# Kernel tuning notes

Measured on AMD Instinct MI355X. Metric: run time of the kernel, lower is better.

## Reference

```python
import jax, jax.numpy as jnp
import numpy as np
import math

D_MODEL = 1024
N_HEADS = 16
SLOT_DIM = 64
N_SLOTS = 1024
TOP_K = 2
LN_EPS = 1e-5


def setup_inputs() -> dict:
    key = jax.random.key(0)
    ks = jax.random.split(key, 8)
    x = jax.random.normal(ks[0], (4, 2048, D_MODEL), dtype=jnp.float32)
    ln_gamma = jnp.ones((D_MODEL,), jnp.float32)
    ln_beta = jnp.zeros((D_MODEL,), jnp.float32)
    q_w = jax.random.normal(ks[1], (N_HEADS * SLOT_DIM, D_MODEL), jnp.float32) / math.sqrt(D_MODEL)
    q_b = jnp.zeros((N_HEADS * SLOT_DIM,), jnp.float32)
    slot_signatures = jax.random.normal(ks[2], (N_HEADS, N_SLOTS, SLOT_DIM), jnp.float32) * 0.5
    slot_values = jax.random.normal(ks[3], (N_HEADS, N_SLOTS, SLOT_DIM), jnp.float32) * 0.02
    out_w = jax.random.normal(ks[4], (D_MODEL, N_HEADS * SLOT_DIM), jnp.float32) / math.sqrt(N_HEADS * SLOT_DIM)
    out_b = jnp.zeros((D_MODEL,), jnp.float32)
    temperature = jnp.ones((1,), jnp.float32)
    return {"x": x, "ln_gamma": ln_gamma, "ln_beta": ln_beta, "q_w": q_w, "q_b": q_b,
            "slot_signatures": slot_signatures, "slot_values": slot_values,
            "out_w": out_w, "out_b": out_b, "temperature": temperature}


def _ternary_ste(sig):
    # forward = {-1,0,+1} quantization; backward = identity (straight-through)
    q = jnp.where(sig > 0.3, 1.0, jnp.where(sig < -0.3, -1.0, 0.0))
    return sig + jax.lax.stop_gradient(q - sig)


def reference(x, ln_gamma, ln_beta, q_w, q_b, slot_signatures, slot_values, out_w, out_b, temperature):
    B, T, D = x.shape
    # LayerNorm
    mean = jnp.mean(x, axis=-1, keepdims=True)
    var = jnp.var(x, axis=-1, keepdims=True)
    x_norm = (x - mean) * jax.lax.rsqrt(var + LN_EPS) * ln_gamma + ln_beta
    # Query projection -> [B, T, H, slot_dim]
    q = (x_norm @ q_w.T + q_b).reshape(B, T, N_HEADS, SLOT_DIM)
    sigs = _ternary_ste(slot_signatures)  # [H, S, d]
    scores = jnp.einsum('bthd,hsd->bths', q, sigs)
    scores = scores / (temperature * math.sqrt(SLOT_DIM))  # [B, T, H, S]
    # top-k routing
    topk_scores, slot_idx = jax.lax.top_k(scores, TOP_K)  # [B, T, H, K]
    weights = jax.nn.softmax(topk_scores, axis=-1)
    # gather selected slot values: [B, T, H, K, d]
    h_idx = jnp.arange(N_HEADS)[None, None, :, None]
    selected = slot_values[h_idx, slot_idx]
    read = jnp.sum(selected * weights[..., None], axis=3)  # [B, T, H, d]
    read = read.reshape(B, T, N_HEADS * SLOT_DIM)
    out = read @ out_w.T + out_b
    return x + out
```

## Files before the change

kernel.cpp:

```cpp
#include <hip/hip_runtime.h>

typedef unsigned short u16;
typedef unsigned int   u32;
typedef float f32x4  __attribute__((ext_vector_type(4)));
typedef __bf16 bf16x8 __attribute__((ext_vector_type(8)));

__device__ __forceinline__ u16 f2bf(float f){
  u32 u = __float_as_uint(f);
  u += 0x7fffu + ((u >> 16) & 1u);
  return (u16)(u >> 16);
}

__device__ __forceinline__ void gld16(const void* g, void* l){
  __builtin_amdgcn_global_load_lds((const __attribute__((address_space(1))) u32*)g,
                                   (__attribute__((address_space(3))) u32*)l, 16, 0, 0);
}

__global__ __launch_bounds__(256) void convert_kernel(
    const float* __restrict__ qw, const float* __restrict__ ow,
    const float* __restrict__ sg,
    u16* __restrict__ qwb, u16* __restrict__ owb, u16* __restrict__ sgb){
  int i = (blockIdx.x * 256 + threadIdx.x) * 4;
  f32x4 a = *(const f32x4*)(qw + i);
  f32x4 b = *(const f32x4*)(ow + i);
  f32x4 s = *(const f32x4*)(sg + i);
  uint2 pa, pb, ps;
  pa.x = (u32)f2bf(a[0]) | ((u32)f2bf(a[1]) << 16);
  pa.y = (u32)f2bf(a[2]) | ((u32)f2bf(a[3]) << 16);
  pb.x = (u32)f2bf(b[0]) | ((u32)f2bf(b[1]) << 16);
  pb.y = (u32)f2bf(b[2]) | ((u32)f2bf(b[3]) << 16);
  float t0 = (s[0] > 0.3f) ? 1.0f : ((s[0] < -0.3f) ? -1.0f : 0.0f);
  float t1 = (s[1] > 0.3f) ? 1.0f : ((s[1] < -0.3f) ? -1.0f : 0.0f);
  float t2 = (s[2] > 0.3f) ? 1.0f : ((s[2] < -0.3f) ? -1.0f : 0.0f);
  float t3 = (s[3] > 0.3f) ? 1.0f : ((s[3] < -0.3f) ? -1.0f : 0.0f);
  ps.x = (u32)f2bf(t0) | ((u32)f2bf(t1) << 16);
  ps.y = (u32)f2bf(t2) | ((u32)f2bf(t3) << 16);
  *(uint2*)(qwb + i) = pa;
  *(uint2*)(owb + i) = pb;
  *(uint2*)(sgb + i) = ps;
}

__global__ __launch_bounds__(256) void ln_kernel(
    const float* __restrict__ x, const float* __restrict__ g,
    const float* __restrict__ b, u16* __restrict__ xn){
  const int t = blockIdx.x, tid = threadIdx.x;
  f32x4 v = *(const f32x4*)(x + (size_t)t * 1024 + tid * 4);
  float s  = v[0] + v[1] + v[2] + v[3];
  float ss = v[0]*v[0] + v[1]*v[1] + v[2]*v[2] + v[3]*v[3];
  for (int off = 32; off; off >>= 1){
    s  += __shfl_down(s, off);
    ss += __shfl_down(ss, off);
  }
  __shared__ float red[8];
  int w = tid >> 6;
  if ((tid & 63) == 0){ red[w] = s; red[4 + w] = ss; }
  __syncthreads();
  s  = red[0] + red[1] + red[2] + red[3];
  ss = red[4] + red[5] + red[6] + red[7];
  float mean = s * (1.0f / 1024.0f);
  float var  = ss * (1.0f / 1024.0f) - mean * mean;
  float rs   = rsqrtf(var + 1e-5f);
  f32x4 gv = *(const f32x4*)(g + tid * 4);
  f32x4 bv = *(const f32x4*)(b + tid * 4);
  float y0 = (v[0]-mean)*rs*gv[0]+bv[0];
  float y1 = (v[1]-mean)*rs*gv[1]+bv[1];
  float y2 = (v[2]-mean)*rs*gv[2]+bv[2];
  float y3 = (v[3]-mean)*rs*gv[3]+bv[3];
  uint2 pk;
  pk.x = (u32)f2bf(y0) | ((u32)f2bf(y1) << 16);
  pk.y = (u32)f2bf(y2) | ((u32)f2bf(y3) << 16);
  *(uint2*)(xn + (size_t)t * 1024 + tid * 4) = pk;
}

__global__ __launch_bounds__(256, 2) void gemm_bt(
    const u16* __restrict__ A, const u16* __restrict__ B,
    const float* __restrict__ bias, const float* __restrict__ resid,
    float* __restrict__ outf, u16* __restrict__ outb, int mode){
  __shared__ u16 As[2][128 * 64];
  __shared__ u16 Bs[2][128 * 64];
  const int tid = threadIdx.x;
  const int b = blockIdx.x;
  const int m0 = ((b & 7) * 8 + ((b >> 3) & 7)) * 128;
  const int n0 = (b >> 6) * 128;
  const int w = tid >> 6, lane = tid & 63, lm = lane & 15, quad = lane >> 4;
  const int wm = (w & 1) * 64, wn = (w >> 1) * 64;
  const int lr = lane >> 3;
  const int lg = (lane & 7) ^ lr;
  const f32x4 fz = {0.f, 0.f, 0.f, 0.f};
  f32x4 acc[4][4];
  #pragma unroll
  for (int i = 0; i < 4; ++i)
    #pragma unroll
    for (int j = 0; j < 4; ++j) acc[i][j] = fz;

  const u16* gA = A + (size_t)(m0 + w * 32 + lr) * 1024 + lg * 8;
  const u16* gB = B + (size_t)(n0 + w * 32 + lr) * 1024 + lg * 8;
  const int lbase = (w * 32) * 64;
  const int sw = lm & 7;

  auto stage = [&](int kt, int bb){
    #pragma unroll
    for (int sub = 0; sub < 4; ++sub){
      gld16(gA + (size_t)(sub * 8) * 1024 + kt * 64, &As[bb][lbase + sub * 8 * 64]);
      gld16(gB + (size_t)(sub * 8) * 1024 + kt * 64, &Bs[bb][lbase + sub * 8 * 64]);
    }
  };

  stage(0, 0);
  for (int kt = 0; kt < 16; ++kt){
    __syncthreads();
    if (kt < 15) stage(kt + 1, (kt + 1) & 1);
    const u16* as = As[kt & 1];
    const u16* bs = Bs[kt & 1];
    #pragma unroll
    for (int kk = 0; kk < 2; ++kk){
      const int ch = ((quad + kk * 4) ^ sw) * 8;
      bf16x8 afr[4], bfr[4];
      #pragma unroll
      for (int i = 0; i < 4; ++i)
        afr[i] = *(const bf16x8*)(&as[(wm + i * 16 + lm) * 64 + ch]);
      #pragma unroll
      for (int j = 0; j < 4; ++j)
        bfr[j] = *(const bf16x8*)(&bs[(wn + j * 16 + lm) * 64 + ch]);
      #pragma unroll
      for (int i = 0; i < 4; ++i)
        #pragma unroll
        for (int j = 0; j < 4; ++j)
          acc[i][j] = __builtin_amdgcn_mfma_f32_16x16x32_bf16(afr[i], bfr[j], acc[i][j], 0, 0, 0);
    }
  }

  #pragma unroll
  for (int i = 0; i < 4; ++i){
    #pragma unroll
    for (int r = 0; r < 4; ++r){
      int grow = m0 + wm + i * 16 + quad * 4 + r;
      #pragma unroll
      for (int j = 0; j < 4; ++j){
        int gcol = n0 + wn + j * 16 + lm;
        float v = acc[i][j][r] + bias[gcol];
        if (mode){
          v += resid[(size_t)grow * 1024 + gcol];
          outf[(size_t)grow * 1024 + gcol] = v;
        } else {
          outb[(size_t)grow * 1024 + gcol] = f2bf(v);
        }
      }
    }
  }
}

__global__ __launch_bounds__(256) void route_kernel(
    const u16* __restrict__ q, const u16* __restrict__ sig,
    const float* __restrict__ V, const float* __restrict__ temp,
    u16* __restrict__ rd){
  const int h = blockIdx.y;
  const int t0 = blockIdx.x * 128;
  const int tid = threadIdx.x, w = tid >> 6, lane = tid & 63;
  const int lm = lane & 15, quad = lane >> 4;

  __shared__ u16 sbuf[2][128 * 64];
  __shared__ float fw1[128], fw2[128];
  __shared__ int   fi1[128], fi2[128];

  const u16* q0 = q + (size_t)(t0 + w * 32 + lm) * 1024 + h * 64 + quad * 8;
  bf16x8 qf00 = *(const bf16x8*)(q0);
  bf16x8 qf01 = *(const bf16x8*)(q0 + 32);
  bf16x8 qf10 = *(const bf16x8*)(q0 + 16 * 1024);
  bf16x8 qf11 = *(const bf16x8*)(q0 + 16 * 1024 + 32);

  const u16* sigh = sig + (size_t)h * 65536;

  const int lr = lane >> 3, lg = (lane & 7) ^ lr;
  const u16* ssrc = sigh + (size_t)(w * 32 + lr) * 64 + lg * 8;
  auto stage = [&](int t, int bb){
    const u16* s0 = ssrc + (size_t)t * 128 * 64;
    u16* d0 = &sbuf[bb][(w * 32) * 64];
    #pragma unroll
    for (int sub = 0; sub < 4; ++sub)
      gld16(s0 + sub * 8 * 64, d0 + sub * 8 * 64);
  };

  const int base1 = lm * 64 + ((quad ^ (lm & 7)) * 8);
  const int base2 = base1 ^ 32;

  const f32x4 fz4 = {0.f, 0.f, 0.f, 0.f};
  const u32 vq = (u32)(quad * 4);
  float v1a = -3.0e38f, v2a = -3.0e38f, v1b = -3.0e38f, v2b = -3.0e38f;
  u32 b1a = 0, b2a = 0, b1b = 0, b2b = 0;

  stage(0, 0);
  for (int t = 0; t < 8; ++t){
    __syncthreads();
    if (t < 7) stage(t + 1, (t + 1) & 1);
    const u16* buf = sbuf[t & 1];
    #pragma unroll
    for (int g = 0; g < 8; ++g){
      bf16x8 s1 = *(const bf16x8*)(&buf[g * 1024 + base1]);
      bf16x8 s2 = *(const bf16x8*)(&buf[g * 1024 + base2]);
      u32 bt = (u32)(t * 8 + g);
      #pragma unroll
      for (int set = 0; set < 2; ++set){
        f32x4 acc = __builtin_amdgcn_mfma_f32_16x16x32_bf16(s1, set ? qf10 : qf00, fz4, 0, 0, 0);
        acc       = __builtin_amdgcn_mfma_f32_16x16x32_bf16(s2, set ? qf11 : qf01, acc, 0, 0, 0);
        float k0 = __uint_as_float((__float_as_uint(acc[0]) & 0xFFFFFFF0u) | vq);
        float k1 = __uint_as_float((__float_as_uint(acc[1]) & 0xFFFFFFF0u) | (vq + 1u));
        float k2 = __uint_as_float((__float_as_uint(acc[2]) & 0xFFFFFFF0u) | (vq + 2u));
        float k3 = __uint_as_float((__float_as_uint(acc[3]) & 0xFFFFFFF0u) | (vq + 3u));
        float h1 = fmaxf(k0, k1), h2 = fminf(k0, k1);
        float h3 = fmaxf(k2, k3), h4 = fminf(k2, k3);
        float m1 = fmaxf(h1, h3);
        float m2 = __builtin_amdgcn_fmed3f(h1, h3, fmaxf(h2, h4));
        float v1 = set ? v1b : v1a, v2 = set ? v2b : v2a;
        u32   b1 = set ? b1b : b1a, b2 = set ? b2b : b2a;
        u32   cb2 = (m2 > v2) ? bt : b2;
        float c2  = fmaxf(v2, m2);
        u32   nb1 = (m1 > v1) ? bt : b1;
        float n1  = fmaxf(v1, m1);
        float n2  = __builtin_amdgcn_fmed3f(v1, m1, c2);
        u32   nb2 = (n2 == m1) ? bt : ((n2 == v1) ? b1 : cb2);
        if (set){ v1b = n1; b1b = nb1; v2b = n2; b2b = nb2; }
        else    { v1a = n1; b1a = nb1; v2a = n2; b2a = nb2; }
      }
    }
  }

  #pragma unroll
  for (int off = 16; off <= 32; off <<= 1){
    #pragma unroll
    for (int set = 0; set < 2; ++set){
      float v1 = set ? v1b : v1a, v2 = set ? v2b : v2a;
      u32   b1 = set ? b1b : b1a, b2 = set ? b2b : b2a;
      float o1 = __shfl_xor(v1, off);
      float o2 = __shfl_xor(v2, off);
      u32 ob1 = (u32)__shfl_xor((int)b1, off);
      u32 ob2 = (u32)__shfl_xor((int)b2, off);
      u32   cb2 = (o2 > v2) ? ob2 : b2;
      float c2  = fmaxf(v2, o2);
      u32   nb1 = (o1 > v1) ? ob1 : b1;
      float n1  = fmaxf(v1, o1);
      float n2  = __builtin_amdgcn_fmed3f(v1, o1, c2);
      u32   nb2 = (n2 == o1) ? ob1 : ((n2 == v1) ? b1 : cb2);
      if (set){ v1b = n1; b1b = nb1; v2b = n2; b2b = nb2; }
      else    { v1a = n1; b1a = nb1; v2a = n2; b2a = nb2; }
    }
  }

  if (quad == 0){
    float tsc = 1.0f / (temp[0] * 8.0f);
    #pragma unroll
    for (int set = 0; set < 2; ++set){
      float v1 = set ? v1b : v1a, v2 = set ? v2b : v2a;
      u32   b1 = set ? b1b : b1a, b2 = set ? b2b : b2a;
      int tl = w * 32 + set * 16 + lm;
      u32 u1 = __float_as_uint(v1);
      u32 u2 = __float_as_uint(v2);
      float s1 = __uint_as_float(u1 & 0xFFFFFFF0u);
      float s2 = __uint_as_float(u2 & 0xFFFFFFF0u);
      float ex = __expf((s2 - s1) * tsc);
      float iw = 1.0f / (1.0f + ex);
      fw1[tl] = iw; fw2[tl] = ex * iw;
      fi1[tl] = (int)(b1 * 16 + (u1 & 15u));
      fi2[tl] = (int)(b2 * 16 + (u2 & 15u));
    }
  }
  __syncthreads();

  int tl = tid >> 1, d0 = (tid & 1) * 32;
  const float* va = V + ((size_t)h * 1024 + fi1[tl]) * 64 + d0;
  const float* vb = V + ((size_t)h * 1024 + fi2[tl]) * 64 + d0;
  float W1 = fw1[tl], W2 = fw2[tl];
  u16* dst = rd + (size_t)(t0 + tl) * 1024 + h * 64 + d0;
  #pragma unroll
  for (int g = 0; g < 4; ++g){
    f32x4 xa = *(const f32x4*)(va + g * 8);
    f32x4 xb = *(const f32x4*)(va + g * 8 + 4);
    f32x4 ya = *(const f32x4*)(vb + g * 8);
    f32x4 yb = *(const f32x4*)(vb + g * 8 + 4);
    uint4 o;
    o.x = (u32)f2bf(W1*xa[0]+W2*ya[0]) | ((u32)f2bf(W1*xa[1]+W2*ya[1]) << 16);
    o.y = (u32)f2bf(W1*xa[2]+W2*ya[2]) | ((u32)f2bf(W1*xa[3]+W2*ya[3]) << 16);
    o.z = (u32)f2bf(W1*xb[0]+W2*yb[0]) | ((u32)f2bf(W1*xb[1]+W2*yb[1]) << 16);
    o.w = (u32)f2bf(W1*xb[2]+W2*yb[2]) | ((u32)f2bf(W1*xb[3]+W2*yb[3]) << 16);
    *(uint4*)(dst + g * 8) = o;
  }
}

extern "C" void kernel_launch(void* const* d_in, const int* in_sizes, int n_in,
                              void* d_out, int out_size, void* d_ws, size_t ws_size,
                              hipStream_t stream){
  const float* x    = (const float*)d_in[0];
  const float* lng  = (const float*)d_in[1];
  const float* lnb  = (const float*)d_in[2];
  const float* qw   = (const float*)d_in[3];
  const float* qb   = (const float*)d_in[4];
  const float* sig  = (const float*)d_in[5];
  const float* sv   = (const float*)d_in[6];
  const float* ow   = (const float*)d_in[7];
  const float* ob   = (const float*)d_in[8];
  const float* temp = (const float*)d_in[9];
  float* out = (float*)d_out;

  char* ws = (char*)d_ws;
  u16* xn   = (u16*)(ws);
  u16* qwb  = (u16*)(ws + 16777216);
  u16* owb  = (u16*)(ws + 16777216 + 2097152);
  u16* sgb  = (u16*)(ws + 16777216 + 2 * 2097152);
  u16* qb16 = (u16*)(ws + 16777216 + 3 * 2097152);
  u16* rdb  = xn;

  convert_kernel<<<1024, 256, 0, stream>>>(qw, ow, sig, qwb, owb, sgb);
  ln_kernel<<<8192, 256, 0, stream>>>(x, lng, lnb, xn);
  gemm_bt<<<512, 256, 0, stream>>>(xn, qwb, qb, nullptr, nullptr, qb16, 0);
  route_kernel<<<dim3(64, 16), 256, 0, stream>>>(qb16, sgb, sv, temp, rdb);
  gemm_bt<<<512, 256, 0, stream>>>(rdb, owb, ob, x, out, nullptr, 1);
}
```

Baseline: 217.1 us.

## Split route slots across waves with 32x32 MFMA and make LayerNorm one wave per row

The routing kernel now gives each wave its own quarter of the slots for 64 tokens, using 32x32x16 bf16 MFMAs. Each wave streams its slots through a private double buffer, synchronized with waitcnt instead of block barriers. The per-wave top-2 results are merged across waves through shared memory before the gather. LayerNorm handles one row per wave using xor-shuffle reductions, which removes the shared-memory reduction and the barrier. The trade-off is more route blocks and a cross-wave merge step, and correctness now depends on the manual waitcnt encodings.

```diff
diff --git a/kernel.cpp b/kernel.cpp
--- a/kernel.cpp
+++ b/kernel.cpp
@@ -3,6 +3,7 @@
 typedef unsigned short u16;
 typedef unsigned int   u32;
 typedef float f32x4  __attribute__((ext_vector_type(4)));
+typedef float f32x16 __attribute__((ext_vector_type(16)));
 typedef __bf16 bf16x8 __attribute__((ext_vector_type(8)));
 
 __device__ __forceinline__ u16 f2bf(float f){
@@ -15,6 +16,10 @@
   __builtin_amdgcn_global_load_lds((const __attribute__((address_space(1))) u32*)g,
                                    (__attribute__((address_space(3))) u32*)l, 16, 0, 0);
 }
+
+#define WAITCNT_VM0   0x0F70
+#define WAITCNT_VM4   0x0F74
+#define WAITCNT_LGKM0 0xC07F
 
 __global__ __launch_bounds__(256) void convert_kernel(
     const float* __restrict__ qw, const float* __restrict__ ow,
@@ -43,33 +48,38 @@
 __global__ __launch_bounds__(256) void ln_kernel(
     const float* __restrict__ x, const float* __restrict__ g,
     const float* __restrict__ b, u16* __restrict__ xn){
-  const int t = blockIdx.x, tid = threadIdx.x;
-  f32x4 v = *(const f32x4*)(x + (size_t)t * 1024 + tid * 4);
-  float s  = v[0] + v[1] + v[2] + v[3];
-  float ss = v[0]*v[0] + v[1]*v[1] + v[2]*v[2] + v[3]*v[3];
+  const int tid = threadIdx.x, lane = tid & 63, w = tid >> 6;
+  const int t = blockIdx.x * 4 + w;
+  const float* xr = x + (size_t)t * 1024;
+  f32x4 v[4];
+  #pragma unroll
+  for (int j = 0; j < 4; ++j) v[j] = *(const f32x4*)(xr + j * 256 + lane * 4);
+  float s = 0.f, ss = 0.f;
+  #pragma unroll
+  for (int j = 0; j < 4; ++j)
+    #pragma unroll
+    for (int e = 0; e < 4; ++e){ s += v[j][e]; ss += v[j][e] * v[j][e]; }
+  #pragma unroll
   for (int off = 32; off; off >>= 1){
-    s  += __shfl_down(s, off);
-    ss += __shfl_down(ss, off);
-  }
-  __shared__ float red[8];
-  int w = tid >> 6;
-  if ((tid & 63) == 0){ red[w] = s; red[4 + w] = ss; }
-  __syncthreads();
-  s  = red[0] + red[1] + red[2] + red[3];
-  ss = red[4] + red[5] + red[6] + red[7];
+    s  += __shfl_xor(s, off);
+    ss += __shfl_xor(ss, off);
+  }
   float mean = s * (1.0f / 1024.0f);
   float var  = ss * (1.0f / 1024.0f) - mean * mean;
   float rs   = rsqrtf(var + 1e-5f);
-  f32x4 gv = *(const f32x4*)(g + tid * 4);
-  f32x4 bv = *(const f32x4*)(b + tid * 4);
-  float y0 = (v[0]-mean)*rs*gv[0]+bv[0];
-  float y1 = (v[1]-mean)*rs*gv[1]+bv[1];
-  float y2 = (v[2]-mean)*rs*gv[2]+bv[2];
-  float y3 = (v[3]-mean)*rs*gv[3]+bv[3];
-  uint2 pk;
-  pk.x = (u32)f2bf(y0) | ((u32)f2bf(y1) << 16);
-  pk.y = (u32)f2bf(y2) | ((u32)f2bf(y3) << 16);
-  *(uint2*)(xn + (size_t)t * 1024 + tid * 4) = pk;
+  #pragma unroll
+  for (int j = 0; j < 4; ++j){
+    f32x4 gv = *(const f32x4*)(g + j * 256 + lane * 4);
+    f32x4 bv = *(const f32x4*)(b + j * 256 + lane * 4);
+    float y0 = (v[j][0]-mean)*rs*gv[0]+bv[0];
+    float y1 = (v[j][1]-mean)*rs*gv[1]+bv[1];
+    float y2 = (v[j][2]-mean)*rs*gv[2]+bv[2];
+    float y3 = (v[j][3]-mean)*rs*gv[3]+bv[3];
+    uint2 pk;
+    pk.x = (u32)f2bf(y0) | ((u32)f2bf(y1) << 16);
+    pk.y = (u32)f2bf(y2) | ((u32)f2bf(y3) << 16);
+    *(uint2*)(xn + (size_t)t * 1024 + j * 256 + lane * 4) = pk;
+  }
 }
 
 __global__ __launch_bounds__(256, 2) void gemm_bt(
@@ -150,129 +160,153 @@
   }
 }
 
+#define MERGE2(V1,I1,V2,I2, o1,oi1,o2,oi2) {                      \
+    u32   cb2 = (o2 > V2) ? oi2 : I2;                             \
+    float c2  = fmaxf(V2, o2);                                    \
+    u32   nb1 = (o1 > V1) ? oi1 : I1;                             \
+    float n1  = fmaxf(V1, o1);                                    \
+    float n2  = __builtin_amdgcn_fmed3f(V1, o1, c2);              \
+    u32   nb2 = (n2 == o1) ? oi1 : ((n2 == V1) ? I1 : cb2);       \
+    V1 = n1; I1 = nb1; V2 = n2; I2 = nb2; }
+
 __global__ __launch_bounds__(256) void route_kernel(
     const u16* __restrict__ q, const u16* __restrict__ sig,
     const float* __restrict__ V, const float* __restrict__ temp,
     u16* __restrict__ rd){
   const int h = blockIdx.y;
-  const int t0 = blockIdx.x * 128;
+  const int t0 = blockIdx.x * 64;
   const int tid = threadIdx.x, w = tid >> 6, lane = tid & 63;
-  const int lm = lane & 15, quad = lane >> 4;
-
-  __shared__ u16 sbuf[2][128 * 64];
-  __shared__ float fw1[128], fw2[128];
-  __shared__ int   fi1[128], fi2[128];
-
-  const u16* q0 = q + (size_t)(t0 + w * 32 + lm) * 1024 + h * 64 + quad * 8;
-  bf16x8 qf00 = *(const bf16x8*)(q0);
-  bf16x8 qf01 = *(const bf16x8*)(q0 + 32);
-  bf16x8 qf10 = *(const bf16x8*)(q0 + 16 * 1024);
-  bf16x8 qf11 = *(const bf16x8*)(q0 + 16 * 1024 + 32);
-
-  const u16* sigh = sig + (size_t)h * 65536;
+  const int col = lane & 31, half = lane >> 5;
+
+  __shared__ u16 sbuf[4][2][32 * 64];
+  __shared__ float sv1[4][64], sv2[4][64];
+  __shared__ u32   si1[4][64], si2[4][64];
+  __shared__ float fw1[64], fw2[64];
+  __shared__ int   fi1[64], fi2[64];
+
+  const u16* q0 = q + (size_t)(t0 + col) * 1024 + h * 64 + half * 8;
+  bf16x8 qa[4], qb[4];
+  #pragma unroll
+  for (int c = 0; c < 4; ++c){
+    qa[c] = *(const bf16x8*)(q0 + c * 16);
+    qb[c] = *(const bf16x8*)(q0 + 32 * 1024 + c * 16);
+  }
+  __builtin_amdgcn_s_waitcnt(WAITCNT_VM0);
 
   const int lr = lane >> 3, lg = (lane & 7) ^ lr;
-  const u16* ssrc = sigh + (size_t)(w * 32 + lr) * 64 + lg * 8;
-  auto stage = [&](int t, int bb){
-    const u16* s0 = ssrc + (size_t)t * 128 * 64;
-    u16* d0 = &sbuf[bb][(w * 32) * 64];
+  const u16* ssrc = sig + (size_t)h * 65536 + (size_t)(w * 256 + lr) * 64 + lg * 8;
+  auto stage = [&](int i, int bb){
+    const u16* s0 = ssrc + (size_t)i * 32 * 64;
+    u16* d0 = &sbuf[w][bb][0];
     #pragma unroll
     for (int sub = 0; sub < 4; ++sub)
       gld16(s0 + sub * 8 * 64, d0 + sub * 8 * 64);
   };
 
-  const int base1 = lm * 64 + ((quad ^ (lm & 7)) * 8);
-  const int base2 = base1 ^ 32;
-
-  const f32x4 fz4 = {0.f, 0.f, 0.f, 0.f};
-  const u32 vq = (u32)(quad * 4);
+  int p[4];
+  #pragma unroll
+  for (int c = 0; c < 4; ++c) p[c] = col * 64 + (((2 * c + half) ^ (col & 7)) * 8);
+
+  const f32x16 fzero = {};
   float v1a = -3.0e38f, v2a = -3.0e38f, v1b = -3.0e38f, v2b = -3.0e38f;
   u32 b1a = 0, b2a = 0, b1b = 0, b2b = 0;
 
   stage(0, 0);
-  for (int t = 0; t < 8; ++t){
-    __syncthreads();
-    if (t < 7) stage(t + 1, (t + 1) & 1);
-    const u16* buf = sbuf[t & 1];
-    #pragma unroll
-    for (int g = 0; g < 8; ++g){
-      bf16x8 s1 = *(const bf16x8*)(&buf[g * 1024 + base1]);
-      bf16x8 s2 = *(const bf16x8*)(&buf[g * 1024 + base2]);
-      u32 bt = (u32)(t * 8 + g);
-      #pragma unroll
-      for (int set = 0; set < 2; ++set){
-        f32x4 acc = __builtin_amdgcn_mfma_f32_16x16x32_bf16(s1, set ? qf10 : qf00, fz4, 0, 0, 0);
-        acc       = __builtin_amdgcn_mfma_f32_16x16x32_bf16(s2, set ? qf11 : qf01, acc, 0, 0, 0);
-        float k0 = __uint_as_float((__float_as_uint(acc[0]) & 0xFFFFFFF0u) | vq);
-        float k1 = __uint_as_float((__float_as_uint(acc[1]) & 0xFFFFFFF0u) | (vq + 1u));
-        float k2 = __uint_as_float((__float_as_uint(acc[2]) & 0xFFFFFFF0u) | (vq + 2u));
-        float k3 = __uint_as_float((__float_as_uint(acc[3]) & 0xFFFFFFF0u) | (vq + 3u));
-        float h1 = fmaxf(k0, k1), h2 = fminf(k0, k1);
-        float h3 = fmaxf(k2, k3), h4 = fminf(k2, k3);
-        float m1 = fmaxf(h1, h3);
-        float m2 = __builtin_amdgcn_fmed3f(h1, h3, fmaxf(h2, h4));
-        float v1 = set ? v1b : v1a, v2 = set ? v2b : v2a;
-        u32   b1 = set ? b1b : b1a, b2 = set ? b2b : b2a;
-        u32   cb2 = (m2 > v2) ? bt : b2;
-        float c2  = fmaxf(v2, m2);
-        u32   nb1 = (m1 > v1) ? bt : b1;
-        float n1  = fmaxf(v1, m1);
-        float n2  = __builtin_amdgcn_fmed3f(v1, m1, c2);
-        u32   nb2 = (n2 == m1) ? bt : ((n2 == v1) ? b1 : cb2);
-        if (set){ v1b = n1; b1b = nb1; v2b = n2; b2b = nb2; }
-        else    { v1a = n1; b1a = nb1; v2a = n2; b2a = nb2; }
-      }
-    }
-  }
-
-  #pragma unroll
-  for (int off = 16; off <= 32; off <<= 1){
+  stage(1, 1);
+  #pragma unroll
+  for (int i = 0; i < 8; ++i){
+    if (i < 7) __builtin_amdgcn_s_waitcnt(WAITCNT_VM4);
+    else       __builtin_amdgcn_s_waitcnt(WAITCNT_VM0);
+    const u16* buf = sbuf[w][i & 1];
+    bf16x8 sf0 = *(const bf16x8*)(&buf[p[0]]);
+    bf16x8 sf1 = *(const bf16x8*)(&buf[p[1]]);
+    bf16x8 sf2 = *(const bf16x8*)(&buf[p[2]]);
+    bf16x8 sf3 = *(const bf16x8*)(&buf[p[3]]);
+    __builtin_amdgcn_s_waitcnt(WAITCNT_LGKM0);
+    if (i < 6) stage(i + 2, i & 1);
+    u32 bt = (u32)i;
     #pragma unroll
     for (int set = 0; set < 2; ++set){
-      float v1 = set ? v1b : v1a, v2 = set ? v2b : v2a;
-      u32   b1 = set ? b1b : b1a, b2 = set ? b2b : b2a;
-      float o1 = __shfl_xor(v1, off);
-      float o2 = __shfl_xor(v2, off);
-      u32 ob1 = (u32)__shfl_xor((int)b1, off);
-      u32 ob2 = (u32)__shfl_xor((int)b2, off);
-      u32   cb2 = (o2 > v2) ? ob2 : b2;
-      float c2  = fmaxf(v2, o2);
-      u32   nb1 = (o1 > v1) ? ob1 : b1;
-      float n1  = fmaxf(v1, o1);
-      float n2  = __builtin_amdgcn_fmed3f(v1, o1, c2);
-      u32   nb2 = (n2 == o1) ? ob1 : ((n2 == v1) ? b1 : cb2);
-      if (set){ v1b = n1; b1b = nb1; v2b = n2; b2b = nb2; }
-      else    { v1a = n1; b1a = nb1; v2a = n2; b2a = nb2; }
-    }
-  }
-
-  if (quad == 0){
+      f32x16 acc;
+      acc = __builtin_amdgcn_mfma_f32_32x32x16_bf16(sf0, set ? qb[0] : qa[0], fzero, 0, 0, 0);
+      acc = __builtin_amdgcn_mfma_f32_32x32x16_bf16(sf1, set ? qb[1] : qa[1], acc, 0, 0, 0);
+      acc = __builtin_amdgcn_mfma_f32_32x32x16_bf16(sf2, set ? qb[2] : qa[2], acc, 0, 0, 0);
+      acc = __builtin_amdgcn_mfma_f32_32x32x16_bf16(sf3, set ? qb[3] : qa[3], acc, 0, 0, 0);
+      float k[16];
+      #pragma unroll
+      for (int r = 0; r < 16; ++r){
+        u32 rk = (u32)((r & 3) + 8 * (r >> 2) + 4 * half);
+        k[r] = __uint_as_float((__float_as_uint(acc[r]) & 0xFFFFFFE0u) | rk);
+      }
+      float h1[8], h2[8];
+      #pragma unroll
+      for (int j = 0; j < 8; ++j){
+        h1[j] = fmaxf(k[2*j], k[2*j+1]);
+        h2[j] = fminf(k[2*j], k[2*j+1]);
+      }
+      float g1[4], g2[4];
+      #pragma unroll
+      for (int j = 0; j < 4; ++j){
+        g1[j] = fmaxf(h1[2*j], h1[2*j+1]);
+        g2[j] = __builtin_amdgcn_fmed3f(h1[2*j], h1[2*j+1], fmaxf(h2[2*j], h2[2*j+1]));
+      }
+      float e1[2], e2[2];
+      #pragma unroll
+      for (int j = 0; j < 2; ++j){
+        e1[j] = fmaxf(g1[2*j], g1[2*j+1]);
+        e2[j] = __builtin_amdgcn_fmed3f(g1[2*j], g1[2*j+1], fmaxf(g2[2*j], g2[2*j+1]));
+      }
+      float m1 = fmaxf(e1[0], e1[1]);
+      float m2 = __builtin_amdgcn_fmed3f(e1[0], e1[1], fmaxf(e2[0], e2[1]));
+      if (set){ MERGE2(v1b, b1b, v2b, b2b, m1, bt, m2, bt); }
+      else    { MERGE2(v1a, b1a, v2a, b2a, m1, bt, m2, bt); }
+    }
+  }
+
+  #pragma unroll
+  for (int set = 0; set < 2; ++set){
+    float v1 = set ? v1b : v1a, v2 = set ? v2b : v2a;
+    u32   b1 = set ? b1b : b1a, b2 = set ? b2b : b2a;
+    float o1 = __shfl_xor(v1, 32);
+    float o2 = __shfl_xor(v2, 32);
+    u32 ob1 = (u32)__shfl_xor((int)b1, 32);
+    u32 ob2 = (u32)__shfl_xor((int)b2, 32);
+    MERGE2(v1, b1, v2, b2, o1, ob1, o2, ob2);
+    if (half == 0){
+      int tk = set * 32 + col;
+      sv1[w][tk] = v1; sv2[w][tk] = v2;
+      si1[w][tk] = (u32)(w * 256) + b1 * 32 + (__float_as_uint(v1) & 31u);
+      si2[w][tk] = (u32)(w * 256) + b2 * 32 + (__float_as_uint(v2) & 31u);
+    }
+  }
+  __syncthreads();
+
+  if (tid < 64){
+    float V1 = sv1[0][tid], V2 = sv2[0][tid];
+    u32   I1 = si1[0][tid], I2 = si2[0][tid];
+    #pragma unroll
+    for (int ws = 1; ws < 4; ++ws){
+      float o1 = sv1[ws][tid], o2 = sv2[ws][tid];
+      u32  oi1 = si1[ws][tid], oi2 = si2[ws][tid];
+      MERGE2(V1, I1, V2, I2, o1, oi1, o2, oi2);
+    }
+    float s1 = __uint_as_float(__float_as_uint(V1) & 0xFFFFFFE0u);
+    float s2 = __uint_as_float(__float_as_uint(V2) & 0xFFFFFFE0u);
     float tsc = 1.0f / (temp[0] * 8.0f);
-    #pragma unroll
-    for (int set = 0; set < 2; ++set){
-      float v1 = set ? v1b : v1a, v2 = set ? v2b : v2a;
-      u32   b1 = set ? b1b : b1a, b2 = set ? b2b : b2a;
-      int tl = w * 32 + set * 16 + lm;
-      u32 u1 = __float_as_uint(v1);
-      u32 u2 = __float_as_uint(v2);
-      float s1 = __uint_as_float(u1 & 0xFFFFFFF0u);
-      float s2 = __uint_as_float(u2 & 0xFFFFFFF0u);
-      float ex = __expf((s2 - s1) * tsc);
-      float iw = 1.0f / (1.0f + ex);
-      fw1[tl] = iw; fw2[tl] = ex * iw;
-      fi1[tl] = (int)(b1 * 16 + (u1 & 15u));
-      fi2[tl] = (int)(b2 * 16 + (u2 & 15u));
-    }
+    float ex = __expf((s2 - s1) * tsc);
+    float iw = 1.0f / (1.0f + ex);
+    fw1[tid] = iw; fw2[tid] = ex * iw;
+    fi1[tid] = (int)I1; fi2[tid] = (int)I2;
   }
   __syncthreads();
 
-  int tl = tid >> 1, d0 = (tid & 1) * 32;
+  int tl = tid >> 2, d0 = (tid & 3) * 16;
   const float* va = V + ((size_t)h * 1024 + fi1[tl]) * 64 + d0;
   const float* vb = V + ((size_t)h * 1024 + fi2[tl]) * 64 + d0;
   float W1 = fw1[tl], W2 = fw2[tl];
   u16* dst = rd + (size_t)(t0 + tl) * 1024 + h * 64 + d0;
   #pragma unroll
-  for (int g = 0; g < 4; ++g){
+  for (int g = 0; g < 2; ++g){
     f32x4 xa = *(const f32x4*)(va + g * 8);
     f32x4 xb = *(const f32x4*)(va + g * 8 + 4);
     f32x4 ya = *(const f32x4*)(vb + g * 8);
@@ -310,8 +344,8 @@
   u16* rdb  = xn;
 
   convert_kernel<<<1024, 256, 0, stream>>>(qw, ow, sig, qwb, owb, sgb);
-  ln_kernel<<<8192, 256, 0, stream>>>(x, lng, lnb, xn);
+  ln_kernel<<<2048, 256, 0, stream>>>(x, lng, lnb, xn);
   gemm_bt<<<512, 256, 0, stream>>>(xn, qwb, qb, nullptr, nullptr, qb16, 0);
-  route_kernel<<<dim3(64, 16), 256, 0, stream>>>(qb16, sgb, sv, temp, rdb);
+  route_kernel<<<dim3(128, 16), 256, 0, stream>>>(qb16, sgb, sv, temp, rdb);
   gemm_bt<<<512, 256, 0, stream>>>(rdb, owb, ob, x, out, nullptr, 1);
 }
```

After: 210.7 us. 1.03x faster.
